# Performance work log

Hardware: AMD Instinct MI355X
Metric: run time of the kernel (lower is better)

## Reference

```python
import jax, jax.numpy as jnp
import numpy as np
from jax import lax

IMG = 1280
VAR0, VAR1 = 0.1, 0.2          # SSD decode variances
CONF_T = 0.7                    # confidence threshold
NMS_T = 0.4                     # IoU threshold
K = 1000                        # fixed NMS candidate budget (jit-friendly)
MIN_SIZES = [[16, 32], [64, 128], [256, 512]]
STEPS = [8, 16, 32]


def make_priors():
    """Vectorized priorbox: [cx, cy, w, h] normalized to [0,1]. N = 67200."""
    out = []
    for ms, s in zip(MIN_SIZES, STEPS):
        f = IMG // s
        ii, jj = np.meshgrid(np.arange(f), np.arange(f), indexing='ij')
        cx = (jj + 0.5) * s / IMG
        cy = (ii + 0.5) * s / IMG
        per_m = [np.stack([cx, cy, np.full_like(cx, m / IMG, dtype=np.float64),
                           np.full_like(cx, m / IMG, dtype=np.float64)], axis=-1)
                 for m in ms]
        a = np.stack(per_m, axis=2)  # [f, f, n_min_sizes, 4] -> matches (i, j, min_size) loop order
        out.append(a.reshape(-1, 4))
    return np.concatenate(out, axis=0).astype(np.float32)


def setup_inputs() -> dict:
    key = jax.random.key(0)
    k1, k2, k3 = jax.random.split(key, 3)
    N = 67200
    loc = jax.random.normal(k1, (1, N, 4), dtype=jnp.float32)
    conf = jax.random.normal(k2, (1, N, 2), dtype=jnp.float32)
    land = jax.random.normal(k3, (1, N, 10), dtype=jnp.float32)
    priors = jnp.asarray(make_priors())
    return {"loc": loc, "conf": conf, "land": land, "priors": priors}


def _decode_boxes(loc, priors):
    # center-form decode then convert to corner form (x1,y1,x2,y2)
    xy = priors[:, :2] + loc[:, :2] * VAR0 * priors[:, 2:]
    wh = priors[:, 2:] * jnp.exp(loc[:, 2:] * VAR1)
    x1y1 = xy - wh * 0.5
    return jnp.concatenate([x1y1, x1y1 + wh], axis=-1)


def _decode_landm(land, priors):
    l = land.reshape(-1, 5, 2)  # 5 landmark points
    pts = priors[:, None, :2] + l * VAR0 * priors[:, None, 2:]
    return pts.reshape(-1, 10)


def _pairwise_iou(b):
    # b: [K, 4] corner-form
    area = (b[:, 2] - b[:, 0]) * (b[:, 3] - b[:, 1])
    lt = jnp.maximum(b[:, None, :2], b[None, :, :2])
    rb = jnp.minimum(b[:, None, 2:], b[None, :, 2:])
    wh = jnp.clip(rb - lt, 0.0)
    inter = wh[..., 0] * wh[..., 1]
    return inter / (area[:, None] + area[None, :] - inter + 1e-12)


def reference(loc, conf, land, priors):
    scores_all = jax.nn.softmax(conf[0], axis=-1)[:, 1]          # [N]
    boxes_all = _decode_boxes(loc[0], priors) * IMG              # [N, 4]
    landms_all = _decode_landm(land[0], priors) * IMG            # [N, 10]

    # threshold (torch.where) + fixed-size top-K selection for jit
    masked = jnp.where(scores_all > CONF_T, scores_all, -jnp.inf)
    top_s, idx = lax.top_k(masked, K)                            # sorted descending
    b = boxes_all[idx]
    lm = landms_all[idx]
    s = scores_all[idx]
    valid = top_s > CONF_T                                       # slots that passed threshold

    # greedy NMS over score-sorted candidates
    iou = _pairwise_iou(b)                                       # [K, K]
    ar = jnp.arange(K)

    def body(i, keep):
        sup = (iou[i] > NMS_T) & (ar > i) & keep[i]
        return keep & ~sup

    keep = lax.fori_loop(0, K, body, valid)

    boxes_out = jnp.where(keep[:, None], b, 0.0)
    scores_out = jnp.where(keep, s, 0.0)
    landms_out = jnp.where(keep[:, None], lm, 0.0)
    return boxes_out, scores_out, landms_out
```

## Files before the change

### kernel.cpp

```cpp
#include <hip/hip_runtime.h>
#include <stdint.h>

#define N_ANCH 67200
#define KCAP   1000
#define CONF_THR 0.7f
#define NMS_THR  0.4f

#define BUCK_BASE 0x3F333333u
#define BUCK_SHIFT 10
#define NBUCK 5120
#define CAPG 4096

#define MID_BLKS 32
#define SUP_BLKS 63

#define OFF_CTR   0
#define OFF_HIST  64
#define OFF_FILL  20544
#define OFF_LIST  41024
#define OFF_GKEYS 578624
#define OFF_SCORE 611392
#define OFF_BOX   615488
#define OFF_LM    631872
#define OFF_SUP   672832

__device__ inline unsigned long long shfl_xor_u64(unsigned long long v, int m) {
    unsigned int lo = (unsigned int)__shfl_xor((int)(v & 0xffffffffull), m, 64);
    unsigned int hi = (unsigned int)__shfl_xor((int)(v >> 32), m, 64);
    return ((unsigned long long)hi << 32) | lo;
}

__device__ inline int bucket_of(unsigned int sb) {
    return min((int)((sb - BUCK_BASE) >> BUCK_SHIFT), NBUCK - 1);
}

__device__ inline void findcut_and_scan(int* sufx, int* swsum, int* sB,
                                        int tid, int lane, int wv) {
    if (tid < 64) {
        int acc = 0, B = 0;
        bool found = false;
        for (int t = 0; t < NBUCK / 64 && !found; ++t) {
            int base = NBUCK - 64 * (t + 1);
            int c = sufx[base + lane];
            int ssum = c;
#pragma unroll
            for (int off = 1; off < 64; off <<= 1)
                ssum += __shfl_xor(ssum, off, 64);
            if (acc + ssum >= KCAP) {
                for (int l = 63; l >= 0; --l) {
                    int cl = (int)__builtin_amdgcn_readlane((unsigned int)c, l);
                    if (acc + cl >= KCAP) { B = base + l; found = true; break; }
                    acc += cl;
                }
            } else {
                acc += ssum;
            }
        }
        if (lane == 0) *sB = found ? B : 0;
    }
    __syncthreads();
    int c[5];
#pragma unroll
    for (int k = 0; k < 5; ++k)
        c[k] = sufx[NBUCK - 1 - (tid * 5 + k)];
    int tsum = c[0] + c[1] + c[2] + c[3] + c[4];
    int inc = tsum;
#pragma unroll
    for (int off = 1; off < 64; off <<= 1) {
        int n = __shfl_up(inc, off, 64);
        if (lane >= off) inc += n;
    }
    if (lane == 63) swsum[wv] = inc;
    __syncthreads();
    if (tid < 16) {
        int v = swsum[tid];
        int s = v;
#pragma unroll
        for (int off = 1; off < 16; off <<= 1) {
            int n = __shfl_up(s, off, 64);
            if (tid >= off) s += n;
        }
        swsum[tid] = s - v;
    }
    __syncthreads();
    int run = swsum[wv] + inc - tsum;
#pragma unroll
    for (int k = 0; k < 5; ++k) {
        sufx[NBUCK - 1 - (tid * 5 + k)] = run;
        run += c[k];
    }
    __syncthreads();
}

__global__ __launch_bounds__(1024) void k_zero(int* __restrict__ ctr,
                                               int* __restrict__ hist,
                                               int* __restrict__ gfill) {
    int tid = threadIdx.x;
    if (tid < 16) ctr[tid] = 0;
    for (int t = tid; t < NBUCK; t += 1024) { hist[t] = 0; gfill[t] = 0; }
}

__global__ __launch_bounds__(256) void k_front(const float* __restrict__ conf,
                                               unsigned long long* __restrict__ list,
                                               int* __restrict__ hist,
                                               int* __restrict__ ctr) {
    int t = blockIdx.x * 256 + threadIdx.x;
    int lane = threadIdx.x & 63;
    int a0 = t * 2;
    bool p0 = false, p1 = false;
    unsigned long long k0 = 0ull, k1 = 0ull;
    if (a0 < N_ANCH) {
        float4 c = reinterpret_cast<const float4*>(conf)[t];
        {
            float mx = fmaxf(c.x, c.y);
            float e0 = expf(c.x - mx), e1 = expf(c.y - mx);
            float s = e1 / (e0 + e1);
            if (s > CONF_THR) {
                p0 = true;
                k0 = ((unsigned long long)__float_as_uint(s) << 32)
                   | (unsigned int)(0xFFFFFFFFu - (unsigned int)a0);
            }
        }
        {
            float mx = fmaxf(c.z, c.w);
            float e0 = expf(c.z - mx), e1 = expf(c.w - mx);
            float s = e1 / (e0 + e1);
            if (s > CONF_THR) {
                p1 = true;
                k1 = ((unsigned long long)__float_as_uint(s) << 32)
                   | (unsigned int)(0xFFFFFFFFu - (unsigned int)(a0 + 1));
            }
        }
    }
    unsigned long long m0 = __ballot(p0);
    unsigned long long m1 = __ballot(p1);
    int n0 = (int)__popcll(m0), n1 = (int)__popcll(m1);
    int base = 0;
    if ((n0 + n1) > 0) {
        if (lane == 0) base = atomicAdd(&ctr[0], n0 + n1);
        base = __shfl(base, 0, 64);
        unsigned long long below = (1ull << lane) - 1ull;
        if (p0) {
            list[base + (int)__popcll(m0 & below)] = k0;
            atomicAdd(&hist[bucket_of((unsigned int)(k0 >> 32))], 1);
        }
        if (p1) {
            list[base + n0 + (int)__popcll(m1 & below)] = k1;
            atomicAdd(&hist[bucket_of((unsigned int)(k1 >> 32))], 1);
        }
    }
}

__global__ __launch_bounds__(1024) void k_midrank(
        const unsigned long long* __restrict__ list,
        const int* __restrict__ hist,
        int* __restrict__ gfill,
        unsigned long long* __restrict__ gkeys,
        int* __restrict__ ctr,
        const float* __restrict__ loc,
        const float* __restrict__ land,
        const float* __restrict__ priors,
        float* __restrict__ sel_score,
        float* __restrict__ sel_box,
        float* __restrict__ sel_lm) {
#pragma clang fp contract(off)
    __shared__ int sufx[NBUCK];
    __shared__ int swsum[16];
    __shared__ int sB;
    __shared__ int slast;
    int tid = threadIdx.x, lane = tid & 63, wv = tid >> 6;
    for (int t = tid; t < NBUCK; t += 1024) sufx[t] = hist[t];
    __syncthreads();
    findcut_and_scan(sufx, swsum, &sB, tid, lane, wv);
    int B = sB;
    int M = min(ctr[0], N_ANCH);

    for (int p = blockIdx.x * 1024 + tid; p < M; p += MID_BLKS * 1024) {
        unsigned long long k = list[p];
        int b = bucket_of((unsigned int)(k >> 32));
        if (b >= B) {
            int off = atomicAdd(&gfill[b], 1);
            int slot = sufx[b] + off;
            if (slot < CAPG) gkeys[slot] = k;
        }
    }
    __syncthreads();
    if (tid == 0) {
        __threadfence();
        int old = atomicAdd(&ctr[1], 1);
        slast = (old == MID_BLKS - 1);
    }
    __syncthreads();
    if (!slast) return;
    if (tid == 0) __threadfence();
    __syncthreads();

    int S = min((B > 0) ? sufx[B - 1] : M, CAPG);
    for (int s = tid; s < S; s += 1024) {
        unsigned long long key = gkeys[s];
        unsigned int sb = (unsigned int)(key >> 32);
        int b = bucket_of(sb);
        int seg0 = sufx[b];
        int segn = gfill[b];
        int within = 0;
        for (int t = 0; t < segn && seg0 + t < CAPG; ++t)
            within += (gkeys[seg0 + t] > key) ? 1 : 0;
        int r = seg0 + within;
        if (r < KCAP) {
            unsigned int a = 0xFFFFFFFFu - (unsigned int)(key & 0xFFFFFFFFull);
            sel_score[r] = __uint_as_float(sb);
            float pcx = priors[a*4+0], pcy = priors[a*4+1];
            float pw  = priors[a*4+2], ph  = priors[a*4+3];
            float l0 = loc[a*4+0], l1 = loc[a*4+1], l2 = loc[a*4+2], l3 = loc[a*4+3];
            float cx = pcx + (l0 * 0.1f) * pw;
            float cy = pcy + (l1 * 0.1f) * ph;
            float w  = pw * expf(l2 * 0.2f);
            float h2 = ph * expf(l3 * 0.2f);
            float x1 = cx - w * 0.5f;
            float y1 = cy - h2 * 0.5f;
            sel_box[r*4+0] = x1 * 1280.0f;
            sel_box[r*4+1] = y1 * 1280.0f;
            sel_box[r*4+2] = (x1 + w) * 1280.0f;
            sel_box[r*4+3] = (y1 + h2) * 1280.0f;
#pragma unroll
            for (int q = 0; q < 5; ++q) {
                float lx = land[a*10 + 2*q + 0];
                float ly = land[a*10 + 2*q + 1];
                sel_lm[r*10 + 2*q + 0] = (pcx + (lx * 0.1f) * pw) * 1280.0f;
                sel_lm[r*10 + 2*q + 1] = (pcy + (ly * 0.1f) * ph) * 1280.0f;
            }
        }
    }
}

__global__ __launch_bounds__(1024) void k_supscan(
        const float* __restrict__ sel_box,
        const float* __restrict__ sel_score,
        const float* __restrict__ sel_lm,
        int* __restrict__ ctr,
        unsigned long long* __restrict__ sup,
        float* __restrict__ out) {
#pragma clang fp contract(off)
    __shared__ unsigned long long sup_r[1024][16];
    __shared__ unsigned long long mshare[16];
    __shared__ unsigned long long keep_final[16];
    __shared__ int slast;
    int tid = threadIdx.x;
    int wave = tid >> 6, lane = tid & 63;
    int V = min(ctr[0], KCAP);

    {
        int i = blockIdx.x * 16 + wave;
        if (i < KCAP) {
            bool irow = (i < V);
            float ax1 = 0.f, ay1 = 0.f, ax2 = 0.f, ay2 = 0.f, aarea = 0.f;
            if (irow) {
                ax1 = sel_box[i*4+0]; ay1 = sel_box[i*4+1];
                ax2 = sel_box[i*4+2]; ay2 = sel_box[i*4+3];
                aarea = (ax2 - ax1) * (ay2 - ay1);
            }
            for (int g = 0; g < 16; ++g) {
                int j = g * 64 + lane;
                bool pred = false;
                if (irow && j < V && j > i) {
                    float4 b = reinterpret_cast<const float4*>(sel_box)[j];
                    float barea = (b.z - b.x) * (b.w - b.y);
                    float ltx = fmaxf(ax1, b.x), lty = fmaxf(ay1, b.y);
                    float rbx = fminf(ax2, b.z), rby = fminf(ay2, b.w);
                    float wx = fmaxf(rbx - ltx, 0.0f);
                    float wy = fmaxf(rby - lty, 0.0f);
                    float inter = wx * wy;
                    float iou = inter / (aarea + barea - inter + 1e-12f);
                    pred = iou > NMS_THR;
                }
                unsigned long long mask = __ballot(pred);
                if (lane == 0) sup[i*16 + g] = mask;
            }
        }
    }
    __syncthreads();
    if (tid == 0) {
        __threadfence();
        int old = atomicAdd(&ctr[2], 1);
        slast = (old == SUP_BLKS - 1);
    }
    __syncthreads();
    if (!slast) return;
    if (tid == 0) __threadfence();
    __syncthreads();

    for (int idx = tid; idx < KCAP * 16; idx += 1024) {
        int r = idx >> 4, w = idx & 15;
        sup_r[r][w ^ (r & 15)] = sup[idx];
    }
    if (tid < 24 * 16) {
        int r = 1000 + (tid >> 4), w = tid & 15;
        sup_r[r][w ^ (r & 15)] = 0ull;
    }
    unsigned long long kw;
    {
        int lo = wave * 64;
        kw = (V >= lo + 64) ? ~0ull : (V <= lo ? 0ull : ((1ull << (V - lo)) - 1ull));
    }
    __syncthreads();

    for (int c = 0; c < 16; ++c) {
        if (wave == c) {
            unsigned long long drow = sup_r[c*64 + lane][c ^ (lane & 15)];
            unsigned int dlo = (unsigned int)drow;
            unsigned int dhi = (unsigned int)(drow >> 32);
            unsigned long long nz = __ballot(drow != 0ull);
            unsigned long long m = kw;
            unsigned long long todo = m & nz;
            while (todo) {
                int i = (int)__builtin_ctzll(todo);
                i = __builtin_amdgcn_readfirstlane(i);
                unsigned long long di =
                    (((unsigned long long)(unsigned int)__builtin_amdgcn_readlane(dhi, i)) << 32)
                  |  (unsigned long long)(unsigned int)__builtin_amdgcn_readlane(dlo, i);
                m &= ~di;
                todo &= ~di;
                todo &= todo - 1ull;
            }
            kw = m;
            if (lane == 0) mshare[c] = m;
        }
        __syncthreads();
        if (wave > c) {
            unsigned long long m = mshare[c];
            unsigned long long contrib = ((m >> lane) & 1ull)
                ? sup_r[c*64 + lane][wave ^ (lane & 15)] : 0ull;
            if (__ballot(contrib != 0ull) != 0ull) {
#pragma unroll
                for (int off = 1; off < 64; off <<= 1)
                    contrib |= shfl_xor_u64(contrib, off);
                kw &= ~contrib;
            }
        }
    }
    if (lane == 0) keep_final[wave] = kw;
    __syncthreads();

    for (int s = tid; s < KCAP; s += 1024) {
        bool kept = ((keep_final[s >> 6] >> (s & 63)) & 1ull) != 0ull;
        float4 b = make_float4(0.f, 0.f, 0.f, 0.f);
        float sc = 0.f;
        if (kept) {
            b  = reinterpret_cast<const float4*>(sel_box)[s];
            sc = sel_score[s];
        }
        reinterpret_cast<float4*>(out)[s] = b;
        out[4000 + s] = sc;
#pragma unroll
        for (int q = 0; q < 10; ++q)
            out[5000 + s*10 + q] = kept ? sel_lm[s*10 + q] : 0.f;
    }
}

extern "C" void kernel_launch(void* const* d_in, const int* in_sizes, int n_in,
                              void* d_out, int out_size, void* d_ws, size_t ws_size,
                              hipStream_t stream) {
    const float* loc    = (const float*)d_in[0];
    const float* conf   = (const float*)d_in[1];
    const float* land   = (const float*)d_in[2];
    const float* priors = (const float*)d_in[3];
    float* out = (float*)d_out;
    char* ws = (char*)d_ws;

    int* ctr                     = (int*)(ws + OFF_CTR);
    int* hist                    = (int*)(ws + OFF_HIST);
    int* gfill                   = (int*)(ws + OFF_FILL);
    unsigned long long* list     = (unsigned long long*)(ws + OFF_LIST);
    unsigned long long* gkeys    = (unsigned long long*)(ws + OFF_GKEYS);
    float* sel_score             = (float*)(ws + OFF_SCORE);
    float* sel_box               = (float*)(ws + OFF_BOX);
    float* sel_lm                = (float*)(ws + OFF_LM);
    unsigned long long* sup      = (unsigned long long*)(ws + OFF_SUP);

    int nfb = (N_ANCH / 2 + 255) / 256;
    k_zero<<<1, 1024, 0, stream>>>(ctr, hist, gfill);
    k_front<<<nfb, 256, 0, stream>>>(conf, list, hist, ctr);
    k_midrank<<<MID_BLKS, 1024, 0, stream>>>(list, hist, gfill, gkeys, ctr,
                                             loc, land, priors,
                                             sel_score, sel_box, sel_lm);
    k_supscan<<<SUP_BLKS, 1024, 0, stream>>>(sel_box, sel_score, sel_lm, ctr,
                                             sup, out);
}
```

Measured before the change: 60.30 us.

## Fuse rank/decode and suppression-scan kernels into one cooperative kernel

Merges the midrank and supscan kernels into a single cooperative launch of 63 blocks. The last block to finish scattering performs the rank/decode step and raises a flag, and all other blocks spin on that flag before building the IoU suppression matrix. The aim is to remove one kernel launch and its inter-kernel gap. In exchange, 62 blocks sit idle during the serial decode phase, and correctness depends on every block being co-resident. The shared-memory histogram and the suppression matrix now share a union, and the matrix load uses 128-bit reads.

```diff
diff --git a/kernel.cpp b/kernel.cpp
--- a/kernel.cpp
+++ b/kernel.cpp
@@ -11,8 +11,7 @@
 #define NBUCK 5120
 #define CAPG 4096
 
-#define MID_BLKS 32
-#define SUP_BLKS 63
+#define FUS_BLKS 63
 
 #define OFF_CTR   0
 #define OFF_HIST  64
@@ -151,7 +150,7 @@
     }
 }
 
-__global__ __launch_bounds__(1024) void k_midrank(
+__global__ __launch_bounds__(1024) void k_fused(
         const unsigned long long* __restrict__ list,
         const int* __restrict__ hist,
         int* __restrict__ gfill,
@@ -162,25 +161,34 @@
         const float* __restrict__ priors,
         float* __restrict__ sel_score,
         float* __restrict__ sel_box,
-        float* __restrict__ sel_lm) {
+        float* __restrict__ sel_lm,
+        unsigned long long* __restrict__ sup,
+        float* __restrict__ out) {
 #pragma clang fp contract(off)
-    __shared__ int sufx[NBUCK];
+    __shared__ union {
+        int sufx[NBUCK];
+        unsigned long long sup_r[1024][16];
+    } u;
     __shared__ int swsum[16];
     __shared__ int sB;
     __shared__ int slast;
-    int tid = threadIdx.x, lane = tid & 63, wv = tid >> 6;
-    for (int t = tid; t < NBUCK; t += 1024) sufx[t] = hist[t];
-    __syncthreads();
-    findcut_and_scan(sufx, swsum, &sB, tid, lane, wv);
+    __shared__ unsigned long long mshare[16];
+    __shared__ unsigned long long keep_final[16];
+    int tid = threadIdx.x, lane = tid & 63, wave = tid >> 6;
+    int bid = blockIdx.x;
+    int M = min(ctr[0], N_ANCH);
+    int V = min(M, KCAP);
+
+    for (int t = tid; t < NBUCK; t += 1024) u.sufx[t] = hist[t];
+    __syncthreads();
+    findcut_and_scan(u.sufx, swsum, &sB, tid, lane, wave);
     int B = sB;
-    int M = min(ctr[0], N_ANCH);
-
-    for (int p = blockIdx.x * 1024 + tid; p < M; p += MID_BLKS * 1024) {
+    for (int p = bid * 1024 + tid; p < M; p += FUS_BLKS * 1024) {
         unsigned long long k = list[p];
         int b = bucket_of((unsigned int)(k >> 32));
         if (b >= B) {
             int off = atomicAdd(&gfill[b], 1);
-            int slot = sufx[b] + off;
+            int slot = u.sufx[b] + off;
             if (slot < CAPG) gkeys[slot] = k;
         }
     }
@@ -188,69 +196,66 @@
     if (tid == 0) {
         __threadfence();
         int old = atomicAdd(&ctr[1], 1);
-        slast = (old == MID_BLKS - 1);
-    }
-    __syncthreads();
-    if (!slast) return;
-    if (tid == 0) __threadfence();
-    __syncthreads();
-
-    int S = min((B > 0) ? sufx[B - 1] : M, CAPG);
-    for (int s = tid; s < S; s += 1024) {
-        unsigned long long key = gkeys[s];
-        unsigned int sb = (unsigned int)(key >> 32);
-        int b = bucket_of(sb);
-        int seg0 = sufx[b];
-        int segn = gfill[b];
-        int within = 0;
-        for (int t = 0; t < segn && seg0 + t < CAPG; ++t)
-            within += (gkeys[seg0 + t] > key) ? 1 : 0;
-        int r = seg0 + within;
-        if (r < KCAP) {
-            unsigned int a = 0xFFFFFFFFu - (unsigned int)(key & 0xFFFFFFFFull);
-            sel_score[r] = __uint_as_float(sb);
-            float pcx = priors[a*4+0], pcy = priors[a*4+1];
-            float pw  = priors[a*4+2], ph  = priors[a*4+3];
-            float l0 = loc[a*4+0], l1 = loc[a*4+1], l2 = loc[a*4+2], l3 = loc[a*4+3];
-            float cx = pcx + (l0 * 0.1f) * pw;
-            float cy = pcy + (l1 * 0.1f) * ph;
-            float w  = pw * expf(l2 * 0.2f);
-            float h2 = ph * expf(l3 * 0.2f);
-            float x1 = cx - w * 0.5f;
-            float y1 = cy - h2 * 0.5f;
-            sel_box[r*4+0] = x1 * 1280.0f;
-            sel_box[r*4+1] = y1 * 1280.0f;
-            sel_box[r*4+2] = (x1 + w) * 1280.0f;
-            sel_box[r*4+3] = (y1 + h2) * 1280.0f;
-#pragma unroll
-            for (int q = 0; q < 5; ++q) {
-                float lx = land[a*10 + 2*q + 0];
-                float ly = land[a*10 + 2*q + 1];
-                sel_lm[r*10 + 2*q + 0] = (pcx + (lx * 0.1f) * pw) * 1280.0f;
-                sel_lm[r*10 + 2*q + 1] = (pcy + (ly * 0.1f) * ph) * 1280.0f;
-            }
-        }
-    }
-}
-
-__global__ __launch_bounds__(1024) void k_supscan(
-        const float* __restrict__ sel_box,
-        const float* __restrict__ sel_score,
-        const float* __restrict__ sel_lm,
-        int* __restrict__ ctr,
-        unsigned long long* __restrict__ sup,
-        float* __restrict__ out) {
-#pragma clang fp contract(off)
-    __shared__ unsigned long long sup_r[1024][16];
-    __shared__ unsigned long long mshare[16];
-    __shared__ unsigned long long keep_final[16];
-    __shared__ int slast;
-    int tid = threadIdx.x;
-    int wave = tid >> 6, lane = tid & 63;
-    int V = min(ctr[0], KCAP);
+        slast = (old == FUS_BLKS - 1);
+    }
+    __syncthreads();
+
+    int S = min((B > 0) ? u.sufx[B - 1] : M, CAPG);
+
+    if (slast) {
+        if (tid == 0) __threadfence();
+        __syncthreads();
+        for (int s = tid; s < S; s += 1024) {
+            unsigned long long key = gkeys[s];
+            unsigned int sb = (unsigned int)(key >> 32);
+            int b = bucket_of(sb);
+            int seg0 = u.sufx[b];
+            int segn = gfill[b];
+            int within = 0;
+            for (int t = 0; t < segn && seg0 + t < CAPG; ++t)
+                within += (gkeys[seg0 + t] > key) ? 1 : 0;
+            int r = seg0 + within;
+            if (r < KCAP) {
+                unsigned int a = 0xFFFFFFFFu - (unsigned int)(key & 0xFFFFFFFFull);
+                sel_score[r] = __uint_as_float(sb);
+                float pcx = priors[a*4+0], pcy = priors[a*4+1];
+                float pw  = priors[a*4+2], ph  = priors[a*4+3];
+                float l0 = loc[a*4+0], l1 = loc[a*4+1], l2 = loc[a*4+2], l3 = loc[a*4+3];
+                float cx = pcx + (l0 * 0.1f) * pw;
+                float cy = pcy + (l1 * 0.1f) * ph;
+                float w  = pw * expf(l2 * 0.2f);
+                float h2 = ph * expf(l3 * 0.2f);
+                float x1 = cx - w * 0.5f;
+                float y1 = cy - h2 * 0.5f;
+                sel_box[r*4+0] = x1 * 1280.0f;
+                sel_box[r*4+1] = y1 * 1280.0f;
+                sel_box[r*4+2] = (x1 + w) * 1280.0f;
+                sel_box[r*4+3] = (y1 + h2) * 1280.0f;
+#pragma unroll
+                for (int q = 0; q < 5; ++q) {
+                    float lx = land[a*10 + 2*q + 0];
+                    float ly = land[a*10 + 2*q + 1];
+                    sel_lm[r*10 + 2*q + 0] = (pcx + (lx * 0.1f) * pw) * 1280.0f;
+                    sel_lm[r*10 + 2*q + 1] = (pcy + (ly * 0.1f) * ph) * 1280.0f;
+                }
+            }
+        }
+        __syncthreads();
+        if (tid == 0) {
+            __threadfence();
+            atomicExch(&ctr[2], 1);
+        }
+    }
+
+    if (tid == 0) {
+        while (atomicAdd(&ctr[2], 0) == 0)
+            __builtin_amdgcn_s_sleep(8);
+        __threadfence();
+    }
+    __syncthreads();
 
     {
-        int i = blockIdx.x * 16 + wave;
+        int i = bid * 16 + wave;
         if (i < KCAP) {
             bool irow = (i < V);
             float ax1 = 0.f, ay1 = 0.f, ax2 = 0.f, ay2 = 0.f, aarea = 0.f;
@@ -281,21 +286,27 @@
     __syncthreads();
     if (tid == 0) {
         __threadfence();
-        int old = atomicAdd(&ctr[2], 1);
-        slast = (old == SUP_BLKS - 1);
+        int old = atomicAdd(&ctr[3], 1);
+        slast = (old == FUS_BLKS - 1);
     }
     __syncthreads();
     if (!slast) return;
     if (tid == 0) __threadfence();
     __syncthreads();
 
-    for (int idx = tid; idx < KCAP * 16; idx += 1024) {
-        int r = idx >> 4, w = idx & 15;
-        sup_r[r][w ^ (r & 15)] = sup[idx];
+    {
+        const ulonglong2* sup2 = reinterpret_cast<const ulonglong2*>(sup);
+        for (int idx = tid; idx < KCAP * 8; idx += 1024) {
+            ulonglong2 v = sup2[idx];
+            int e0 = idx * 2;
+            int r = e0 >> 4, w0 = e0 & 15;
+            u.sup_r[r][w0 ^ (r & 15)] = v.x;
+            u.sup_r[r][(w0 + 1) ^ (r & 15)] = v.y;
+        }
     }
     if (tid < 24 * 16) {
         int r = 1000 + (tid >> 4), w = tid & 15;
-        sup_r[r][w ^ (r & 15)] = 0ull;
+        u.sup_r[r][w ^ (r & 15)] = 0ull;
     }
     unsigned long long kw;
     {
@@ -306,7 +317,7 @@
 
     for (int c = 0; c < 16; ++c) {
         if (wave == c) {
-            unsigned long long drow = sup_r[c*64 + lane][c ^ (lane & 15)];
+            unsigned long long drow = u.sup_r[c*64 + lane][c ^ (lane & 15)];
             unsigned int dlo = (unsigned int)drow;
             unsigned int dhi = (unsigned int)(drow >> 32);
             unsigned long long nz = __ballot(drow != 0ull);
@@ -329,7 +340,7 @@
         if (wave > c) {
             unsigned long long m = mshare[c];
             unsigned long long contrib = ((m >> lane) & 1ull)
-                ? sup_r[c*64 + lane][wave ^ (lane & 15)] : 0ull;
+                ? u.sup_r[c*64 + lane][wave ^ (lane & 15)] : 0ull;
             if (__ballot(contrib != 0ull) != 0ull) {
 #pragma unroll
                 for (int off = 1; off < 64; off <<= 1)
@@ -380,9 +391,11 @@
     int nfb = (N_ANCH / 2 + 255) / 256;
     k_zero<<<1, 1024, 0, stream>>>(ctr, hist, gfill);
     k_front<<<nfb, 256, 0, stream>>>(conf, list, hist, ctr);
-    k_midrank<<<MID_BLKS, 1024, 0, stream>>>(list, hist, gfill, gkeys, ctr,
-                                             loc, land, priors,
-                                             sel_score, sel_box, sel_lm);
-    k_supscan<<<SUP_BLKS, 1024, 0, stream>>>(sel_box, sel_score, sel_lm, ctr,
-                                             sup, out);
-}
+
+    void* args[] = { (void*)&list, (void*)&hist, (void*)&gfill, (void*)&gkeys,
+                     (void*)&ctr, (void*)&loc, (void*)&land, (void*)&priors,
+                     (void*)&sel_score, (void*)&sel_box, (void*)&sel_lm,
+                     (void*)&sup, (void*)&out };
+    hipLaunchCooperativeKernel((const void*)k_fused, dim3(FUS_BLKS), dim3(1024),
+                               args, 0, stream);
+}
```

After: 79.97 us. +32.6%, slower.

## Replace global histogram atomics with per-block histograms and drop zero kernel

Applied to the files above, without the earlier changes.

The front kernel now builds a coarse 192-bucket score histogram in shared memory per block and writes candidates into per-block list segments, removing global atomics on the counter and histogram. The mid-rank kernel sums the per-block histograms itself and scans the coarse buckets with a single wave, replacing the 5120-bucket scan. The separate zeroing kernel is removed because front block 0 resets the fill and sync counters, saving one launch. The suppression-matrix copy into shared memory now uses 128-bit loads. Coarser buckets can put more keys into the cut bucket, which makes the in-bucket rank loop longer.

```diff
diff --git a/kernel.cpp b/kernel.cpp
--- a/kernel.cpp
+++ b/kernel.cpp
@@ -7,22 +7,24 @@
 #define NMS_THR  0.4f
 
 #define BUCK_BASE 0x3F333333u
-#define BUCK_SHIFT 10
-#define NBUCK 5120
+#define CSHIFT 15
+#define NBUCKC 192
 #define CAPG 4096
 
+#define NFB 132
 #define MID_BLKS 32
 #define SUP_BLKS 63
 
 #define OFF_CTR   0
-#define OFF_HIST  64
-#define OFF_FILL  20544
-#define OFF_LIST  41024
-#define OFF_GKEYS 578624
-#define OFF_SCORE 611392
-#define OFF_BOX   615488
-#define OFF_LM    631872
-#define OFF_SUP   672832
+#define OFF_BCNT  64
+#define OFF_BHIST 640
+#define OFF_FILL  102016
+#define OFF_LIST  102784
+#define OFF_GKEYS 643456
+#define OFF_SCORE 676224
+#define OFF_BOX   680320
+#define OFF_LM    696704
+#define OFF_SUP   737664
 
 __device__ inline unsigned long long shfl_xor_u64(unsigned long long v, int m) {
     unsigned int lo = (unsigned int)__shfl_xor((int)(v & 0xffffffffull), m, 64);
@@ -31,17 +33,112 @@
 }
 
 __device__ inline int bucket_of(unsigned int sb) {
-    return min((int)((sb - BUCK_BASE) >> BUCK_SHIFT), NBUCK - 1);
-}
-
-__device__ inline void findcut_and_scan(int* sufx, int* swsum, int* sB,
-                                        int tid, int lane, int wv) {
+    return min((int)((sb - BUCK_BASE) >> CSHIFT), NBUCKC - 1);
+}
+
+__global__ __launch_bounds__(256) void k_front(const float* __restrict__ conf,
+                                               unsigned long long* __restrict__ list,
+                                               int* __restrict__ bhist,
+                                               int* __restrict__ bcnt,
+                                               int* __restrict__ gfill,
+                                               int* __restrict__ ctr) {
+    __shared__ int lhist[NBUCKC];
+    __shared__ int lcnt;
+    int tid = threadIdx.x, lane = tid & 63;
+    int blk = blockIdx.x;
+    if (tid < NBUCKC) lhist[tid] = 0;
+    if (tid == 0) lcnt = 0;
+    __syncthreads();
+
+    int p = blk * 256 + tid;
+    int a0 = p * 2;
+    bool p0 = false, p1 = false;
+    unsigned long long k0 = 0ull, k1 = 0ull;
+    if (a0 < N_ANCH) {
+        float4 c = reinterpret_cast<const float4*>(conf)[p];
+        {
+            float mx = fmaxf(c.x, c.y);
+            float e0 = expf(c.x - mx), e1 = expf(c.y - mx);
+            float s = e1 / (e0 + e1);
+            if (s > CONF_THR) {
+                p0 = true;
+                k0 = ((unsigned long long)__float_as_uint(s) << 32)
+                   | (unsigned int)(0xFFFFFFFFu - (unsigned int)a0);
+            }
+        }
+        {
+            float mx = fmaxf(c.z, c.w);
+            float e0 = expf(c.z - mx), e1 = expf(c.w - mx);
+            float s = e1 / (e0 + e1);
+            if (s > CONF_THR) {
+                p1 = true;
+                k1 = ((unsigned long long)__float_as_uint(s) << 32)
+                   | (unsigned int)(0xFFFFFFFFu - (unsigned int)(a0 + 1));
+            }
+        }
+    }
+    unsigned long long m0 = __ballot(p0);
+    unsigned long long m1 = __ballot(p1);
+    int n0 = (int)__popcll(m0), n1 = (int)__popcll(m1);
+    int base = 0;
+    if (lane == 0 && (n0 + n1) > 0) base = atomicAdd(&lcnt, n0 + n1);
+    base = __shfl(base, 0, 64);
+    unsigned long long below = (1ull << lane) - 1ull;
+    int gbase = blk * 512;
+    if (p0) {
+        list[gbase + base + (int)__popcll(m0 & below)] = k0;
+        atomicAdd(&lhist[bucket_of((unsigned int)(k0 >> 32))], 1);
+    }
+    if (p1) {
+        list[gbase + base + n0 + (int)__popcll(m1 & below)] = k1;
+        atomicAdd(&lhist[bucket_of((unsigned int)(k1 >> 32))], 1);
+    }
+    __syncthreads();
+    if (tid < NBUCKC) bhist[blk * NBUCKC + tid] = lhist[tid];
+    if (tid == 0) bcnt[blk] = lcnt;
+    if (blk == 0) {
+        if (tid < NBUCKC) gfill[tid] = 0;
+        if (tid == 192) ctr[1] = 0;
+        if (tid == 193) ctr[2] = 0;
+    }
+}
+
+__global__ __launch_bounds__(1024) void k_midrank(
+        const unsigned long long* __restrict__ list,
+        const int* __restrict__ bhist,
+        const int* __restrict__ bcnt,
+        int* __restrict__ gfill,
+        unsigned long long* __restrict__ gkeys,
+        int* __restrict__ ctr,
+        const float* __restrict__ loc,
+        const float* __restrict__ land,
+        const float* __restrict__ priors,
+        float* __restrict__ sel_score,
+        float* __restrict__ sel_box,
+        float* __restrict__ sel_lm) {
+#pragma clang fp contract(off)
+    __shared__ int chist[NBUCKC];
+    __shared__ int scnt[NFB];
+    __shared__ int sB, sM;
+    __shared__ int slast;
+    int tid = threadIdx.x, lane = tid & 63;
+    int bid = blockIdx.x;
+
+    if (tid < NFB) scnt[tid] = bcnt[tid];
+    if (tid < NBUCKC) {
+        int s = 0;
+#pragma unroll 4
+        for (int j = 0; j < NFB; ++j) s += bhist[j * NBUCKC + tid];
+        chist[tid] = s;
+    }
+    __syncthreads();
+
     if (tid < 64) {
         int acc = 0, B = 0;
         bool found = false;
-        for (int t = 0; t < NBUCK / 64 && !found; ++t) {
-            int base = NBUCK - 64 * (t + 1);
-            int c = sufx[base + lane];
+        for (int t = 0; t < NBUCKC / 64 && !found; ++t) {
+            int base = NBUCKC - 64 * (t + 1);
+            int c = chist[base + lane];
             int ssum = c;
 #pragma unroll
             for (int off = 1; off < 64; off <<= 1)
@@ -56,132 +153,41 @@
                 acc += ssum;
             }
         }
-        if (lane == 0) *sB = found ? B : 0;
-    }
-    __syncthreads();
-    int c[5];
-#pragma unroll
-    for (int k = 0; k < 5; ++k)
-        c[k] = sufx[NBUCK - 1 - (tid * 5 + k)];
-    int tsum = c[0] + c[1] + c[2] + c[3] + c[4];
-    int inc = tsum;
-#pragma unroll
-    for (int off = 1; off < 64; off <<= 1) {
-        int n = __shfl_up(inc, off, 64);
-        if (lane >= off) inc += n;
-    }
-    if (lane == 63) swsum[wv] = inc;
-    __syncthreads();
-    if (tid < 16) {
-        int v = swsum[tid];
-        int s = v;
-#pragma unroll
-        for (int off = 1; off < 16; off <<= 1) {
-            int n = __shfl_up(s, off, 64);
-            if (tid >= off) s += n;
-        }
-        swsum[tid] = s - v;
-    }
-    __syncthreads();
-    int run = swsum[wv] + inc - tsum;
-#pragma unroll
-    for (int k = 0; k < 5; ++k) {
-        sufx[NBUCK - 1 - (tid * 5 + k)] = run;
-        run += c[k];
-    }
-    __syncthreads();
-}
-
-__global__ __launch_bounds__(1024) void k_zero(int* __restrict__ ctr,
-                                               int* __restrict__ hist,
-                                               int* __restrict__ gfill) {
-    int tid = threadIdx.x;
-    if (tid < 16) ctr[tid] = 0;
-    for (int t = tid; t < NBUCK; t += 1024) { hist[t] = 0; gfill[t] = 0; }
-}
-
-__global__ __launch_bounds__(256) void k_front(const float* __restrict__ conf,
-                                               unsigned long long* __restrict__ list,
-                                               int* __restrict__ hist,
-                                               int* __restrict__ ctr) {
-    int t = blockIdx.x * 256 + threadIdx.x;
-    int lane = threadIdx.x & 63;
-    int a0 = t * 2;
-    bool p0 = false, p1 = false;
-    unsigned long long k0 = 0ull, k1 = 0ull;
-    if (a0 < N_ANCH) {
-        float4 c = reinterpret_cast<const float4*>(conf)[t];
-        {
-            float mx = fmaxf(c.x, c.y);
-            float e0 = expf(c.x - mx), e1 = expf(c.y - mx);
-            float s = e1 / (e0 + e1);
-            if (s > CONF_THR) {
-                p0 = true;
-                k0 = ((unsigned long long)__float_as_uint(s) << 32)
-                   | (unsigned int)(0xFFFFFFFFu - (unsigned int)a0);
-            }
-        }
-        {
-            float mx = fmaxf(c.z, c.w);
-            float e0 = expf(c.z - mx), e1 = expf(c.w - mx);
-            float s = e1 / (e0 + e1);
-            if (s > CONF_THR) {
-                p1 = true;
-                k1 = ((unsigned long long)__float_as_uint(s) << 32)
-                   | (unsigned int)(0xFFFFFFFFu - (unsigned int)(a0 + 1));
-            }
-        }
-    }
-    unsigned long long m0 = __ballot(p0);
-    unsigned long long m1 = __ballot(p1);
-    int n0 = (int)__popcll(m0), n1 = (int)__popcll(m1);
-    int base = 0;
-    if ((n0 + n1) > 0) {
-        if (lane == 0) base = atomicAdd(&ctr[0], n0 + n1);
-        base = __shfl(base, 0, 64);
-        unsigned long long below = (1ull << lane) - 1ull;
-        if (p0) {
-            list[base + (int)__popcll(m0 & below)] = k0;
-            atomicAdd(&hist[bucket_of((unsigned int)(k0 >> 32))], 1);
-        }
-        if (p1) {
-            list[base + n0 + (int)__popcll(m1 & below)] = k1;
-            atomicAdd(&hist[bucket_of((unsigned int)(k1 >> 32))], 1);
-        }
-    }
-}
-
-__global__ __launch_bounds__(1024) void k_midrank(
-        const unsigned long long* __restrict__ list,
-        const int* __restrict__ hist,
-        int* __restrict__ gfill,
-        unsigned long long* __restrict__ gkeys,
-        int* __restrict__ ctr,
-        const float* __restrict__ loc,
-        const float* __restrict__ land,
-        const float* __restrict__ priors,
-        float* __restrict__ sel_score,
-        float* __restrict__ sel_box,
-        float* __restrict__ sel_lm) {
-#pragma clang fp contract(off)
-    __shared__ int sufx[NBUCK];
-    __shared__ int swsum[16];
-    __shared__ int sB;
-    __shared__ int slast;
-    int tid = threadIdx.x, lane = tid & 63, wv = tid >> 6;
-    for (int t = tid; t < NBUCK; t += 1024) sufx[t] = hist[t];
-    __syncthreads();
-    findcut_and_scan(sufx, swsum, &sB, tid, lane, wv);
+        if (lane == 0) sB = found ? B : 0;
+    }
+    __syncthreads();
+    if (tid < 64) {
+        int acc = 0;
+        for (int t = 0; t < NBUCKC / 64; ++t) {
+            int base = NBUCKC - 64 * (t + 1);
+            int c = chist[base + lane];
+            int inc = c;
+#pragma unroll
+            for (int off = 1; off < 64; off <<= 1) {
+                int n = __shfl_down(inc, off, 64);
+                if (lane + off < 64) inc += n;
+            }
+            chist[base + lane] = acc + inc - c;
+            acc += __shfl(inc, 0, 64);
+        }
+        if (lane == 0) sM = acc;
+    }
+    __syncthreads();
     int B = sB;
-    int M = min(ctr[0], N_ANCH);
-
-    for (int p = blockIdx.x * 1024 + tid; p < M; p += MID_BLKS * 1024) {
-        unsigned long long k = list[p];
-        int b = bucket_of((unsigned int)(k >> 32));
-        if (b >= B) {
-            int off = atomicAdd(&gfill[b], 1);
-            int slot = sufx[b] + off;
-            if (slot < CAPG) gkeys[slot] = k;
+    int M = sM;
+    int V = min(M, KCAP);
+    if (bid == 0 && tid == 0) ctr[0] = V;
+
+    for (int slot = bid * 1024 + tid; slot < NFB * 512; slot += MID_BLKS * 1024) {
+        int seg = slot >> 9, off = slot & 511;
+        if (off < scnt[seg]) {
+            unsigned long long k = list[slot];
+            int b = bucket_of((unsigned int)(k >> 32));
+            if (b >= B) {
+                int o = atomicAdd(&gfill[b], 1);
+                int pos = chist[b] + o;
+                if (pos < CAPG) gkeys[pos] = k;
+            }
         }
     }
     __syncthreads();
@@ -195,12 +201,12 @@
     if (tid == 0) __threadfence();
     __syncthreads();
 
-    int S = min((B > 0) ? sufx[B - 1] : M, CAPG);
+    int S = min((B > 0) ? chist[B - 1] : M, CAPG);
     for (int s = tid; s < S; s += 1024) {
         unsigned long long key = gkeys[s];
         unsigned int sb = (unsigned int)(key >> 32);
         int b = bucket_of(sb);
-        int seg0 = sufx[b];
+        int seg0 = chist[b];
         int segn = gfill[b];
         int within = 0;
         for (int t = 0; t < segn && seg0 + t < CAPG; ++t)
@@ -289,9 +295,15 @@
     if (tid == 0) __threadfence();
     __syncthreads();
 
-    for (int idx = tid; idx < KCAP * 16; idx += 1024) {
-        int r = idx >> 4, w = idx & 15;
-        sup_r[r][w ^ (r & 15)] = sup[idx];
+    {
+        const ulonglong2* sup2 = reinterpret_cast<const ulonglong2*>(sup);
+        for (int idx = tid; idx < KCAP * 8; idx += 1024) {
+            ulonglong2 v = sup2[idx];
+            int e0 = idx * 2;
+            int r = e0 >> 4, w0 = e0 & 15;
+            sup_r[r][w0 ^ (r & 15)] = v.x;
+            sup_r[r][(w0 + 1) ^ (r & 15)] = v.y;
+        }
     }
     if (tid < 24 * 16) {
         int r = 1000 + (tid >> 4), w = tid & 15;
@@ -368,7 +380,8 @@
     char* ws = (char*)d_ws;
 
     int* ctr                     = (int*)(ws + OFF_CTR);
-    int* hist                    = (int*)(ws + OFF_HIST);
+    int* bcnt                    = (int*)(ws + OFF_BCNT);
+    int* bhist                   = (int*)(ws + OFF_BHIST);
     int* gfill                   = (int*)(ws + OFF_FILL);
     unsigned long long* list     = (unsigned long long*)(ws + OFF_LIST);
     unsigned long long* gkeys    = (unsigned long long*)(ws + OFF_GKEYS);
@@ -377,11 +390,9 @@
     float* sel_lm                = (float*)(ws + OFF_LM);
     unsigned long long* sup      = (unsigned long long*)(ws + OFF_SUP);
 
-    int nfb = (N_ANCH / 2 + 255) / 256;
-    k_zero<<<1, 1024, 0, stream>>>(ctr, hist, gfill);
-    k_front<<<nfb, 256, 0, stream>>>(conf, list, hist, ctr);
-    k_midrank<<<MID_BLKS, 1024, 0, stream>>>(list, hist, gfill, gkeys, ctr,
-                                             loc, land, priors,
+    k_front<<<NFB, 256, 0, stream>>>(conf, list, bhist, bcnt, gfill, ctr);
+    k_midrank<<<MID_BLKS, 1024, 0, stream>>>(list, bhist, bcnt, gfill, gkeys,
+                                             ctr, loc, land, priors,
                                              sel_score, sel_box, sel_lm);
     k_supscan<<<SUP_BLKS, 1024, 0, stream>>>(sel_box, sel_score, sel_lm, ctr,
                                              sup, out);
```

After: 68.00 us. +12.8%, slower.
